# Optimization experiments

Measured on AMD Instinct MI355X. Metric: run time of the kernel, lower is better.

The kernel has to match this reference:

```python
import jax, jax.numpy as jnp
import numpy as np

EPS = 1e-5      # BatchNorm eps
K_STEPS = 10    # explicit PDE time steps
DT = 0.2
CDX = 1.0
CDY = 1.0


def dwconv(x, w, b):
    # depthwise 3x3 conv, padding 1 (nn.Conv2d groups=C). x:[B,C,H,W], w:[C,1,3,3]
    y = jax.lax.conv_general_dilated(
        x, w, window_strides=(1, 1), padding=((1, 1), (1, 1)),
        dimension_numbers=('NCHW', 'OIHW', 'NCHW'),
        feature_group_count=x.shape[1])
    return y + b[None, :, None, None]


def bn(x, s, b, m, v):
    # inference-mode BatchNorm2d with running stats
    inv = s * jax.lax.rsqrt(v + EPS)
    return (x - m[None, :, None, None]) * inv[None, :, None, None] + b[None, :, None, None]


def setup_inputs() -> dict:
    key = jax.random.key(0)
    ks = jax.random.split(key, 7)
    B, C, H, W = 32, 256, 56, 56
    x = jax.random.normal(ks[0], (B, C, H, W), jnp.float32)
    # small scale keeps the K-step explicit integrator numerically tame
    conv_w = jax.random.normal(ks[1], (4, C, 1, 3, 3), jnp.float32) * 0.05
    conv_b = jax.random.normal(ks[2], (4, C), jnp.float32) * 0.05
    bn_scale = jax.random.uniform(ks[3], (5, C), jnp.float32, 0.5, 1.5)
    bn_bias = jax.random.normal(ks[4], (5, C), jnp.float32) * 0.1
    bn_mean = jax.random.normal(ks[5], (5, C), jnp.float32) * 0.1
    bn_var = jax.random.uniform(ks[6], (5, C), jnp.float32, 0.5, 1.5)
    return {"x": x, "conv_w": conv_w, "conv_b": conv_b, "bn_scale": bn_scale,
            "bn_bias": bn_bias, "bn_mean": bn_mean, "bn_var": bn_var}


def reference(x, conv_w, conv_b, bn_scale, bn_bias, bn_mean, bn_var):
    f = x
    h = x  # init_h = nn.Identity (cell_type='default'), init_h0_h=False
    # advection velocities u, v and diffusivities Dx, Dy, all computed once from h
    u = jax.nn.relu(bn(dwconv(h, conv_w[0], conv_b[0]), bn_scale[0], bn_bias[0], bn_mean[0], bn_var[0]))
    v = jax.nn.relu(bn(dwconv(h, conv_w[1], conv_b[1]), bn_scale[1], bn_bias[1], bn_mean[1], bn_var[1]))
    Dx = CDX * jax.nn.sigmoid(bn(dwconv(h, conv_w[2], conv_b[2]), bn_scale[2], bn_bias[2], bn_mean[2], bn_var[2]))
    Dy = CDY * jax.nn.sigmoid(bn(dwconv(h, conv_w[3], conv_b[3]), bn_scale[3], bn_bias[3], bn_mean[3], bn_var[3]))

    def step(h, _):
        # finite-difference stencil (dx=dy=1), shifts along H (axis 2) and W (axis 3)
        hxp = jnp.roll(h, -1, axis=2)
        hxm = jnp.roll(h, 1, axis=2)
        hyp = jnp.roll(h, -1, axis=3)
        hym = jnp.roll(h, 1, axis=3)
        h_xx = hxp + hxm - 2.0 * h
        h_yy = hyp + hym - 2.0 * h
        h_x = 0.5 * (hxp - hxm)
        h_y = 0.5 * (hyp - hym)
        # explicit Euler: nonlinear diffusion + advection + forcing f (no_f=False)
        h_new = h + DT * (Dx * h_xx + Dy * h_yy + u * h_x + v * h_y + f)
        return h_new, None

    h, _ = jax.lax.scan(step, h, None, length=K_STEPS)
    out = jax.nn.relu(bn(h, bn_scale[4], bn_bias[4], bn_mean[4], bn_var[4]))  # bn_out + relu
    return out
```

## Files before the change

kernel.cpp:

```cpp
#include <hip/hip_runtime.h>

#define K_STEPS 10

typedef float f32x2 __attribute__((ext_vector_type(2)));

__device__ __forceinline__ f32x2 fma2v(f32x2 a, f32x2 b, f32x2 c) {
    return __builtin_elementwise_fma(a, b, c);
}

__global__ __launch_bounds__(448)
__attribute__((amdgpu_waves_per_eu(4, 4)))
void pde_fused10(const float* __restrict__ x,
                 const float* __restrict__ conv_w,
                 const float* __restrict__ conv_b,
                 const float* __restrict__ bn_s,
                 const float* __restrict__ bn_b,
                 const float* __restrict__ bn_m,
                 const float* __restrict__ bn_v,
                 float* __restrict__ out,
                 int C, int pairs)
{
    const float DTc = 0.2f, EPSc = 1e-5f;
    __shared__ f32x2 smem[6500];
    const int tid = threadIdx.x;
    const int bid = blockIdx.x;
    const int ch  = bid % C;
    const size_t base0 = (size_t)bid * 3136;
    const size_t base1 = (size_t)(bid + pairs) * 3136;

    f32x2* xs = smem;
    f32x2* hA = smem + 3364;
    f32x2* hB = smem;

    if (tid < 232) {
        int o;
        if      (tid < 58)  o = tid;
        else if (tid < 116) o = 57 * 58 + (tid - 58);
        else if (tid < 174) o = (tid - 116) * 58;
        else                o = (tid - 174) * 58 + 57;
        xs[o] = (f32x2){0.0f, 0.0f};
    }

    float xv0[7], xv1[7];
    #pragma unroll
    for (int k = 0; k < 7; ++k) xv0[k] = x[base0 + tid + k * 448];
    #pragma unroll
    for (int k = 0; k < 7; ++k) xv1[k] = x[base1 + tid + k * 448];

    float wj[4][9], cbj[4];
    #pragma unroll
    for (int j = 0; j < 4; ++j) {
        #pragma unroll
        for (int tt = 0; tt < 9; ++tt) wj[j][tt] = conv_w[(j * C + ch) * 9 + tt];
        cbj[j] = conv_b[j * C + ch];
    }
    float g[5], be[5];
    #pragma unroll
    for (int j = 0; j < 5; ++j) {
        float inv = bn_s[j * C + ch] * rsqrtf(bn_v[j * C + ch] + EPSc);
        g[j]  = inv;
        be[j] = bn_b[j * C + ch] - bn_m[j * C + ch] * inv;
    }

    #pragma unroll
    for (int k = 0; k < 7; ++k) {
        int idx = tid + k * 448;
        int rr = idx / 56, cc = idx - rr * 56;
        xs[(rr + 1) * 58 + (cc + 1)] = (f32x2){xv0[k], xv1[k]};
    }
    __syncthreads();

    const int r  = tid >> 3;
    const int c0 = (tid & 7) * 7;

    f32x2 h[7], F[7], A[7], Xp[7], Xm[7], Yp[7], Ym[7];

    #pragma unroll
    for (int i = 0; i < 7; ++i) {
        f32x2 a0 = (f32x2){cbj[0], cbj[0]};
        f32x2 a1 = (f32x2){cbj[1], cbj[1]};
        f32x2 a2 = (f32x2){cbj[2], cbj[2]};
        f32x2 a3 = (f32x2){cbj[3], cbj[3]};
        f32x2 hv;
        #pragma unroll
        for (int dr = 0; dr < 3; ++dr)
            #pragma unroll
            for (int dc = 0; dc < 3; ++dc) {
                f32x2 xw = xs[(r + dr) * 58 + (c0 + i + dc)];
                if (dr == 1 && dc == 1) hv = xw;
                float w0 = wj[0][dr * 3 + dc], w1 = wj[1][dr * 3 + dc];
                float w2 = wj[2][dr * 3 + dc], w3 = wj[3][dr * 3 + dc];
                a0 = fma2v(xw, (f32x2){w0, w0}, a0);
                a1 = fma2v(xw, (f32x2){w1, w1}, a1);
                a2 = fma2v(xw, (f32x2){w2, w2}, a2);
                a3 = fma2v(xw, (f32x2){w3, w3}, a3);
            }
        float uux = fmaxf(fmaf(a0.x, g[0], be[0]), 0.0f);
        float uuy = fmaxf(fmaf(a0.y, g[0], be[0]), 0.0f);
        float vvx = fmaxf(fmaf(a1.x, g[1], be[1]), 0.0f);
        float vvy = fmaxf(fmaf(a1.y, g[1], be[1]), 0.0f);
        float z2x = fmaf(a2.x, g[2], be[2]), z2y = fmaf(a2.y, g[2], be[2]);
        float z3x = fmaf(a3.x, g[3], be[3]), z3y = fmaf(a3.y, g[3], be[3]);
        float Dxx = 1.0f / (1.0f + __expf(-z2x));
        float Dxy = 1.0f / (1.0f + __expf(-z2y));
        float Dyx = 1.0f / (1.0f + __expf(-z3x));
        float Dyy = 1.0f / (1.0f + __expf(-z3y));
        float Ax = DTc * Dxx, Ay = DTc * Dxy;
        float Bx = DTc * Dyx, By = DTc * Dyy;
        float Ux = 0.5f * DTc * uux, Uy = 0.5f * DTc * uuy;
        float Vx = 0.5f * DTc * vvx, Vy = 0.5f * DTc * vvy;
        h[i]  = hv;
        F[i]  = (f32x2){DTc * hv.x, DTc * hv.y};
        A[i]  = (f32x2){1.0f - 2.0f * Ax - 2.0f * Bx,
                        1.0f - 2.0f * Ay - 2.0f * By};
        Xp[i] = (f32x2){Ax + Ux, Ay + Uy};
        Xm[i] = (f32x2){Ax - Ux, Ay - Uy};
        Yp[i] = (f32x2){Bx + Vx, By + Vy};
        Ym[i] = (f32x2){Bx - Vx, By - Vy};
    }

    const int o_me = r * 56 + c0;
    #pragma unroll
    for (int i = 0; i < 7; ++i) hA[o_me + i] = h[i];
    __syncthreads();

    const int rm = (r == 0)  ? 55 : r - 1;
    const int rp = (r == 55) ? 0  : r + 1;
    const int o_up = rm * 56 + c0;
    const int o_dn = rp * 56 + c0;
    const int o_l  = r * 56 + ((c0 == 0)  ? 55 : c0 - 1);
    const int o_r  = r * 56 + ((c0 == 49) ? 0  : c0 + 7);

    f32x2 *cur = hA, *nxt = hB;
    #pragma unroll
    for (int s = 0; s < K_STEPS; ++s) {
        f32x2 lf = cur[o_l];
        f32x2 rg = cur[o_r];
        f32x2 nh[7];
        #pragma unroll
        for (int i = 0; i < 7; ++i) {
            f32x2 ui = cur[o_up + i];
            f32x2 di = cur[o_dn + i];
            f32x2 hl = (i == 0) ? lf : h[i - 1];
            f32x2 hr = (i == 6) ? rg : h[i + 1];
            f32x2 tv = fma2v(A[i], h[i], F[i]);
            tv = fma2v(Xm[i], ui, tv);
            tv = fma2v(Xp[i], di, tv);
            tv = fma2v(Ym[i], hl, tv);
            tv = fma2v(Yp[i], hr, tv);
            nh[i] = tv;
        }
        #pragma unroll
        for (int i = 0; i < 7; ++i) nxt[o_me + i] = nh[i];
        #pragma unroll
        for (int i = 0; i < 7; ++i) h[i] = nh[i];
        __syncthreads();
        f32x2* t2 = cur; cur = nxt; nxt = t2;
    }

    #pragma unroll
    for (int k = 0; k < 7; ++k) {
        int idx = tid + k * 448;
        f32x2 v = cur[idx];
        out[base0 + idx] = fmaxf(fmaf(v.x, g[4], be[4]), 0.0f);
        out[base1 + idx] = fmaxf(fmaf(v.y, g[4], be[4]), 0.0f);
    }
}

extern "C" void kernel_launch(void* const* d_in, const int* in_sizes, int n_in,
                              void* d_out, int out_size, void* d_ws, size_t ws_size,
                              hipStream_t stream) {
    const float* x  = (const float*)d_in[0];
    const float* cw = (const float*)d_in[1];
    const float* cb = (const float*)d_in[2];
    const float* bs = (const float*)d_in[3];
    const float* bb = (const float*)d_in[4];
    const float* bm = (const float*)d_in[5];
    const float* bv = (const float*)d_in[6];
    float* out = (float*)d_out;

    int C = in_sizes[2] / 4;
    int planes = in_sizes[0] / 3136;
    int pairs = planes / 2;

    pde_fused10<<<pairs, 448, 0, stream>>>(x, cw, cb, bs, bb, bm, bv, out, C, pairs);
}
```

Measured before the change: 150.1 us.

## Pack stencil coefficients in half precision and skip final LDS round-trip

Stores the six per-pixel stencil coefficient arrays as packed half2 instead of float2, which roughly halves their register footprint, and converts them back to float inside each FMA. It drops the shared-memory store and barrier after the last time step and writes the output directly from registers. The launch-bounds hint changes from an explicit waves-per-EU attribute to a min-blocks argument. The extra half-to-float conversions add ALU work per step, the packed FMAs become scalar FMAs, and fp16 rounding of the coefficients reduces precision. Output stores now go from each thread's own row segment rather than a coalesced linear index.

Result: slower. 237.0 us (+57.9%).

```diff
diff --git a/kernel.cpp b/kernel.cpp
--- a/kernel.cpp
+++ b/kernel.cpp
@@ -1,4 +1,5 @@
 #include <hip/hip_runtime.h>
+#include <hip/hip_fp16.h>
 
 #define K_STEPS 10
 
@@ -8,9 +9,8 @@
     return __builtin_elementwise_fma(a, b, c);
 }
 
-__global__ __launch_bounds__(448)
-__attribute__((amdgpu_waves_per_eu(4, 4)))
-void pde_fused10(const float* __restrict__ x,
+__global__ __launch_bounds__(448, 4)
+void pde_fused12(const float* __restrict__ x,
                  const float* __restrict__ conv_w,
                  const float* __restrict__ conv_b,
                  const float* __restrict__ bn_s,
@@ -73,7 +73,8 @@
     const int r  = tid >> 3;
     const int c0 = (tid & 7) * 7;
 
-    f32x2 h[7], F[7], A[7], Xp[7], Xm[7], Yp[7], Ym[7];
+    __half2 cA[7], cXp[7], cXm[7], cYp[7], cYm[7], cF[7];
+    f32x2 h[7];
 
     #pragma unroll
     for (int i = 0; i < 7; ++i) {
@@ -109,14 +110,14 @@
         float Bx = DTc * Dyx, By = DTc * Dyy;
         float Ux = 0.5f * DTc * uux, Uy = 0.5f * DTc * uuy;
         float Vx = 0.5f * DTc * vvx, Vy = 0.5f * DTc * vvy;
-        h[i]  = hv;
-        F[i]  = (f32x2){DTc * hv.x, DTc * hv.y};
-        A[i]  = (f32x2){1.0f - 2.0f * Ax - 2.0f * Bx,
-                        1.0f - 2.0f * Ay - 2.0f * By};
-        Xp[i] = (f32x2){Ax + Ux, Ay + Uy};
-        Xm[i] = (f32x2){Ax - Ux, Ay - Uy};
-        Yp[i] = (f32x2){Bx + Vx, By + Vy};
-        Ym[i] = (f32x2){Bx - Vx, By - Vy};
+        h[i]   = hv;
+        cF[i]  = __floats2half2_rn(DTc * hv.x, DTc * hv.y);
+        cA[i]  = __floats2half2_rn(1.0f - 2.0f * Ax - 2.0f * Bx,
+                                   1.0f - 2.0f * Ay - 2.0f * By);
+        cXp[i] = __floats2half2_rn(Ax + Ux, Ay + Uy);
+        cXm[i] = __floats2half2_rn(Ax - Ux, Ay - Uy);
+        cYp[i] = __floats2half2_rn(Bx + Vx, By + Vy);
+        cYm[i] = __floats2half2_rn(Bx - Vx, By - Vy);
     }
 
     const int o_me = r * 56 + c0;
@@ -143,27 +144,33 @@
             f32x2 di = cur[o_dn + i];
             f32x2 hl = (i == 0) ? lf : h[i - 1];
             f32x2 hr = (i == 6) ? rg : h[i + 1];
-            f32x2 tv = fma2v(A[i], h[i], F[i]);
-            tv = fma2v(Xm[i], ui, tv);
-            tv = fma2v(Xp[i], di, tv);
-            tv = fma2v(Ym[i], hl, tv);
-            tv = fma2v(Yp[i], hr, tv);
-            nh[i] = tv;
+            float tx = fmaf(__half2float(cA[i].x),  h[i].x, __half2float(cF[i].x));
+            float ty = fmaf(__half2float(cA[i].y),  h[i].y, __half2float(cF[i].y));
+            tx = fmaf(__half2float(cXm[i].x), ui.x, tx);
+            ty = fmaf(__half2float(cXm[i].y), ui.y, ty);
+            tx = fmaf(__half2float(cXp[i].x), di.x, tx);
+            ty = fmaf(__half2float(cXp[i].y), di.y, ty);
+            tx = fmaf(__half2float(cYm[i].x), hl.x, tx);
+            ty = fmaf(__half2float(cYm[i].y), hl.y, ty);
+            tx = fmaf(__half2float(cYp[i].x), hr.x, tx);
+            ty = fmaf(__half2float(cYp[i].y), hr.y, ty);
+            nh[i] = (f32x2){tx, ty};
         }
         #pragma unroll
-        for (int i = 0; i < 7; ++i) nxt[o_me + i] = nh[i];
-        #pragma unroll
         for (int i = 0; i < 7; ++i) h[i] = nh[i];
-        __syncthreads();
-        f32x2* t2 = cur; cur = nxt; nxt = t2;
+        if (s < K_STEPS - 1) {
+            #pragma unroll
+            for (int i = 0; i < 7; ++i) nxt[o_me + i] = nh[i];
+            __syncthreads();
+            f32x2* t2 = cur; cur = nxt; nxt = t2;
+        }
     }
 
     #pragma unroll
-    for (int k = 0; k < 7; ++k) {
-        int idx = tid + k * 448;
-        f32x2 v = cur[idx];
-        out[base0 + idx] = fmaxf(fmaf(v.x, g[4], be[4]), 0.0f);
-        out[base1 + idx] = fmaxf(fmaf(v.y, g[4], be[4]), 0.0f);
+    for (int i = 0; i < 7; ++i) {
+        size_t o = (size_t)(r * 56 + c0 + i);
+        out[base0 + o] = fmaxf(fmaf(h[i].x, g[4], be[4]), 0.0f);
+        out[base1 + o] = fmaxf(fmaf(h[i].y, g[4], be[4]), 0.0f);
     }
 }
 
@@ -183,5 +190,5 @@
     int planes = in_sizes[0] / 3136;
     int pairs = planes / 2;
 
-    pde_fused10<<<pairs, 448, 0, stream>>>(x, cw, cb, bs, bb, bm, bv, out, C, pairs);
+    pde_fused12<<<pairs, 448, 0, stream>>>(x, cw, cb, bs, bb, bm, bv, out, C, pairs);
 }
```
